# Optimization experiments

Hardware: AMD Instinct MI355X
Metric: run time of the kernel (lower is better)

Reference implementation:

```python
import jax, jax.numpy as jnp
import numpy as np
from jax import lax

N = 8192            # total ensemble boxes
W_IMG, H_IMG = 1920.0, 1080.0
NUM_MODELS = 5
CLUSTER_IOU = 0.5   # coalesce_boxes threshold


def setup_inputs() -> dict:
    key = jax.random.key(0)
    k1, k2, k3, k4, k5 = jax.random.split(key, 5)
    x1 = jax.random.uniform(k1, (N,)) * (W_IMG - 60.0)
    y1 = jax.random.uniform(k2, (N,)) * (H_IMG - 60.0)
    w = jax.random.uniform(k3, (N,)) * 180.0 + 4.0
    h = jax.random.uniform(k4, (N,)) * 180.0 + 4.0
    boxes = jnp.stack([x1, y1, x1 + w, y1 + h], axis=1)          # [N,4] xyxy
    scores = jax.random.uniform(k5, (N,)) * 0.7 + 0.3            # conf_thres=0.3
    return {"boxes": boxes, "scores": scores, "num_models": NUM_MODELS}


def _edf_forward(boxes, scores, num_models):
    n = boxes.shape[0]
    # clip to image (original also rounds; rounding omitted to keep grads alive)
    x1 = jnp.clip(boxes[:, 0], 0.0, W_IMG)
    y1 = jnp.clip(boxes[:, 1], 0.0, H_IMG)
    x2 = jnp.clip(boxes[:, 2], 0.0, W_IMG)
    y2 = jnp.clip(boxes[:, 3], 0.0, H_IMG)
    # coalesce_boxes processes boxes in descending score order (sort asc, pop)
    order = jnp.argsort(-scores)
    b = jnp.stack([x1, y1, x2, y2], axis=1)[order]               # [N,4]
    s = scores[order]
    bx1, by1, bx2, by2 = b[:, 0], b[:, 1], b[:, 2], b[:, 3]
    area = (bx2 - bx1 + 1.0) * (by2 - by1 + 1.0)
    # pairwise IoU with the +1 convention of bb_intersection_over_union
    ix1 = jnp.maximum(bx1[:, None], bx1[None, :])
    iy1 = jnp.maximum(by1[:, None], by1[None, :])
    ix2 = jnp.minimum(bx2[:, None], bx2[None, :])
    iy2 = jnp.minimum(by2[:, None], by2[None, :])
    inter = jnp.maximum(ix2 - ix1 + 1.0, 0.0) * jnp.maximum(iy2 - iy1 + 1.0, 0.0)
    iou = inter / (area[:, None] + area[None, :] - inter)        # [N,N]
    adj = iou > CLUSTER_IOU
    # greedy clustering: in score order, an unassigned box becomes a cluster
    # head and absorbs every still-unassigned box with IoU(head, j) > 0.5
    def step(cluster, i):
        is_head = cluster[i] < 0
        cluster = jnp.where(is_head & (cluster < 0) & adj[i], i, cluster)
        return cluster, None
    cluster, _ = lax.scan(step, jnp.full((n,), -1, jnp.int32),
                          jnp.arange(n, dtype=jnp.int32))
    counts = jax.ops.segment_sum(jnp.ones((n,), jnp.float32), cluster, num_segments=n)
    # per-group nms() only returns pick[0]: the member with max y2 (ties -> first)
    seg_y2 = jax.ops.segment_max(by2, cluster, num_segments=n)
    idx = jnp.arange(n)
    cand = by2 >= seg_y2[cluster]
    first = jax.ops.segment_min(jnp.where(cand, idx, n), cluster, num_segments=n)
    is_pick = idx == first[cluster]
    # probFinal = sum of group scores; final score = probFinal / num_models
    prob = jax.ops.segment_sum(s, cluster, num_segments=n)
    score_out = prob[cluster] / num_models
    # 'consensus': keep group iff its size >= num_models / 3
    valid = counts >= (num_models / 3.0)
    keep = is_pick & valid[cluster]
    out = jnp.where(keep[:, None],
                    jnp.concatenate([b, score_out[:, None]], axis=1),
                    0.0)                                         # [N,5] padded
    return out, keep


def reference(boxes, scores, num_models):
    return _edf_forward(boxes, scores, num_models)
```

## Files before the change

kernel.cpp:

```cpp
#include <hip/hip_runtime.h>
#include <cstdint>

#define N 8192
#define NT 128
#define RITERS 12
typedef unsigned long long u64;
typedef unsigned int u32;

__device__ inline u64 readlane64(u64 v, int lane) {
  u32 lo = (u32)__builtin_amdgcn_readlane((int)(u32)v, lane);
  u32 hi = (u32)__builtin_amdgcn_readlane((int)(u32)(v >> 32), lane);
  return ((u64)hi << 32) | lo;
}

__global__ __launch_bounds__(256) void k_init(const float* __restrict__ scores,
                                              u64* __restrict__ keys,
                                              int* __restrict__ rank,
                                              int* __restrict__ cnt,
                                              float* __restrict__ prob,
                                              unsigned* __restrict__ y2m,
                                              int* __restrict__ first,
                                              u64* __restrict__ D,
                                              u64* __restrict__ S) {
  int i = blockIdx.x * 256 + threadIdx.x;
  if (i >= N) return;
  float sc = scores[i];
  keys[i] = ((u64)__float_as_uint(sc) << 32) | (unsigned)(0xFFFFFFFFu - (unsigned)i);
  rank[i] = 0;
  cnt[i] = 0;
  prob[i] = 0.0f;
  y2m[i] = 0u;
  first[i] = N;
  if (i < NT) { D[i] = 0ull; S[i] = 0ull; }
}

__global__ __launch_bounds__(256) void k_rank(const u64* __restrict__ keys,
                                              int* __restrict__ rank) {
  __shared__ u64 tile[1024];
  int e = blockIdx.x * 256 + threadIdx.x;
  int j0 = blockIdx.y * 1024;
  for (int t = threadIdx.x; t < 1024; t += 256) tile[t] = keys[j0 + t];
  __syncthreads();
  u64 ke = keys[e];
  int c = 0;
#pragma unroll 8
  for (int k = 0; k < 1024; ++k) c += (tile[k] > ke) ? 1 : 0;
  atomicAdd(&rank[e], c);
}

__global__ __launch_bounds__(256) void k_scatter(const float* __restrict__ boxes,
                                                 const float* __restrict__ scores,
                                                 const int* __restrict__ rank,
                                                 float* __restrict__ bx1s, float* __restrict__ by1s,
                                                 float* __restrict__ bx2s, float* __restrict__ by2s,
                                                 float* __restrict__ ss, float* __restrict__ areas) {
#pragma clang fp contract(off)
  int i = blockIdx.x * 256 + threadIdx.x;
  if (i >= N) return;
  int r = rank[i];
  float x1 = fminf(fmaxf(boxes[i * 4 + 0], 0.0f), 1920.0f);
  float y1 = fminf(fmaxf(boxes[i * 4 + 1], 0.0f), 1080.0f);
  float x2 = fminf(fmaxf(boxes[i * 4 + 2], 0.0f), 1920.0f);
  float y2 = fminf(fmaxf(boxes[i * 4 + 3], 0.0f), 1080.0f);
  bx1s[r] = x1; by1s[r] = y1; bx2s[r] = x2; by2s[r] = y2;
  ss[r] = scores[i];
  areas[r] = (x2 - x1 + 1.0f) * (y2 - y1 + 1.0f);
}

__global__ __launch_bounds__(256) void k_adj(const float* __restrict__ bx1s, const float* __restrict__ by1s,
                                             const float* __restrict__ bx2s, const float* __restrict__ by2s,
                                             const float* __restrict__ areas,
                                             u64* __restrict__ mtile,
                                             u64* __restrict__ mrow) {
#pragma clang fp contract(off)
  __shared__ float jx1[4][64], jy1[4][64], jx2[4][64], jy2[4][64], ja[4][64];
  int w = threadIdx.x >> 6, l = threadIdx.x & 63;
  int p = blockIdx.x * 4 + w;
  int gy = (int)((sqrtf(8.0f * (float)p + 1.0f) - 1.0f) * 0.5f);
  while ((gy + 1) * (gy + 2) / 2 <= p) ++gy;
  while (gy * (gy + 1) / 2 > p) --gy;
  int gx = p - gy * (gy + 1) / 2;

  int j = gx * 64 + l;
  jx1[w][l] = bx1s[j]; jy1[w][l] = by1s[j]; jx2[w][l] = bx2s[j]; jy2[w][l] = by2s[j]; ja[w][l] = areas[j];
  __syncthreads();
  int i = gy * 64 + l;
  float x1 = bx1s[i], y1 = by1s[i], x2 = bx2s[i], y2 = by2s[i], ai = areas[i];
  u64 bits = 0;
#pragma unroll 4
  for (int jj = 0; jj < 64; ++jj) {
    float ix1 = fmaxf(x1, jx1[w][jj]);
    float iy1 = fmaxf(y1, jy1[w][jj]);
    float ix2 = fminf(x2, jx2[w][jj]);
    float iy2 = fminf(y2, jy2[w][jj]);
    float iw = fmaxf(ix2 - ix1 + 1.0f, 0.0f);
    float ih = fmaxf(iy2 - iy1 + 1.0f, 0.0f);
    float inter = iw * ih;
    float uni = (ai + ja[w][jj]) - inter;
    float t = inter + inter;
    bool gt = t > uni;
    bool amb = fabsf(t - uni) <= 1e-6f * uni;
    if (__ballot(amb) != 0ull) {
      float iou = inter / uni;
      if (amb) gt = iou > 0.5f;
    }
    bits |= ((u64)gt) << jj;
  }
  mtile[((size_t)gy * NT + gx) * 64 + l] = bits;
  mrow[(size_t)i * NT + gx] = bits;
  if (gx != gy) {
    u64 tb = 0;
#pragma unroll 8
    for (int c = 0; c < 64; ++c) {
      u64 wb = __ballot((bits >> c) & 1ull);
      tb = (l == c) ? wb : tb;
    }
    mtile[((size_t)gx * NT + gy) * 64 + l] = tb;
    mrow[(size_t)(gx * 64 + l) * NT + gy] = tb;
  }
}

__global__ __launch_bounds__(256) void k_rounds(const u64* __restrict__ mtile,
                                                u64* __restrict__ D,
                                                u64* __restrict__ S) {
  __shared__ u64 Dl[NT], Sl[NT];
  __shared__ u64 bw[3][4];
  __shared__ u64 fD, fU, fE;
  int gy = blockIdx.x;
  int t = threadIdx.x;
  int w = t >> 6, r = t & 63;
  u64 dAA = (w == 0) ? mtile[((size_t)gy * NT + gy) * 64 + r] : 0ull;

  for (int it = 0; it < RITERS; ++it) {
    if (t < NT) Dl[t] = __hip_atomic_load(&D[t], __ATOMIC_RELAXED, __HIP_MEMORY_SCOPE_AGENT);
    else Sl[t - NT] = __hip_atomic_load(&S[t - NT], __ATOMIC_RELAXED, __HIP_MEMORY_SCOPE_AGENT);
    __syncthreads();
    u64 classified = Dl[gy] | Sl[gy];
    if (classified == ~0ull) return;
    bool unk = !((classified >> r) & 1ull);
    u64 anyD = 0, anyU = 0, anyE = 0;
    if (unk) {
      int k0 = 32 * w, k1 = min(k0 + 32, gy + 1);
      for (int k = k0; k < k1; ++k) {
        u64 m = mtile[((size_t)gy * NT + k) * 64 + r];
        if (k == gy) {
          m &= (1ull << r) - 1ull;
          anyD |= m & Dl[k];
          anyU |= m & ~Sl[k];
        } else {
          anyD |= m & Dl[k];
          anyU |= m & ~Sl[k];
          anyE |= m & ~(Sl[k] | Dl[k]);
        }
      }
    }
    u64 bD = __ballot(anyD != 0ull), bU = __ballot(anyU != 0ull), bE = __ballot(anyE != 0ull);
    if (r == 0) { bw[0][w] = bD; bw[1][w] = bU; bw[2][w] = bE; }
    __syncthreads();
    if (t == 0) {
      fD = bw[0][0] | bw[0][1] | bw[0][2] | bw[0][3];
      fU = bw[1][0] | bw[1][1] | bw[1][2] | bw[1][3];
      fE = bw[2][0] | bw[2][1] | bw[2][2] | bw[2][3];
    }
    __syncthreads();
    u64 rD = fD, rU = fU, rE = fE;
    u64 unkb = ~classified;
    if (rE == 0ull) {
      if (w == 0) {
        u64 t0 = unkb & ~rD;
        u64 heads = 0, todo = t0;
        while (todo) {
          int i = __builtin_ctzll(todo);
          heads |= 1ull << i;
          todo &= ~readlane64(dAA, i);
        }
        if (r == 0) {
          if (heads) atomicOr(&D[gy], heads);
          u64 ns = unkb & ~heads;
          if (ns) atomicOr(&S[gy], ns);
        }
      }
      return;
    }
    if (t == 0) {
      u64 newS = unkb & rD;
      u64 newD = unkb & ~rD & ~rU;
      if (newS) atomicOr(&S[gy], newS);
      if (newD) atomicOr(&D[gy], newD);
    }
    __syncthreads();
  }
}

__global__ __launch_bounds__(64, 1) void k_fix(const u64* __restrict__ mrow,
                                               u64* __restrict__ D,
                                               const u64* __restrict__ S) {
  __shared__ int ulist[N];
  int l = threadIdx.x;
  u64 D0 = D[2 * l], D1 = D[2 * l + 1];
  u64 S0 = S[2 * l], S1 = S[2 * l + 1];
  u64 u0 = ~(D0 | S0), u1 = ~(D1 | S1);
  int cnt = __popcll(u0) + __popcll(u1);
  int pre = cnt;
  for (int d = 1; d < 64; d <<= 1) {
    int v = __shfl_up(pre, d);
    if (l >= d) pre += v;
  }
  int M = __shfl(pre, 63);
  int off = pre - cnt;
  {
    u64 v = u0; int o = off;
    while (v) { int b = __builtin_ctzll(v); v &= v - 1; ulist[o++] = l * 128 + b; }
    v = u1;
    while (v) { int b = __builtin_ctzll(v); v &= v - 1; ulist[o++] = l * 128 + 64 + b; }
  }
  __syncthreads();
  if (M > 0) {
    ulong2 ring[8];
    int pj[8];
#pragma unroll
    for (int q = 0; q < 8; ++q) {
      int j = ulist[q < M ? q : M - 1];
      pj[q] = j;
      ring[q] = *(const ulong2*)&mrow[(size_t)j * NT + 2 * l];
    }
    for (int m = 0; m < M; ++m) {
      int slot = m & 7;
      int j = pj[slot];
      ulong2 rv = ring[slot];
      int jt = j >> 6;
      u64 bm = (1ull << (j & 63)) - 1ull;
      u64 m0 = (2 * l < jt) ? ~0ull : ((2 * l == jt) ? bm : 0ull);
      u64 m1 = (2 * l + 1 < jt) ? ~0ull : ((2 * l + 1 == jt) ? bm : 0ull);
      bool hit = ((rv.x & D0 & m0) | (rv.y & D1 & m1)) != 0ull;
      bool head = (__ballot(hit) == 0ull);
      u64 bset = 1ull << (j & 63);
      D0 |= (head && (2 * l == jt)) ? bset : 0ull;
      D1 |= (head && (2 * l + 1 == jt)) ? bset : 0ull;
      int nm = m + 8;
      int j2 = ulist[nm < M ? nm : M - 1];
      pj[slot] = j2;
      ring[slot] = *(const ulong2*)&mrow[(size_t)j2 * NT + 2 * l];
    }
  }
  D[2 * l] = D0;
  D[2 * l + 1] = D1;
}

__global__ __launch_bounds__(256) void k_cluster(const u64* __restrict__ mtile,
                                                 const u64* __restrict__ D,
                                                 const float* __restrict__ ss,
                                                 const float* __restrict__ by2s,
                                                 int* __restrict__ cluster,
                                                 int* __restrict__ cnt,
                                                 float* __restrict__ prob,
                                                 unsigned* __restrict__ y2m) {
  __shared__ u64 hlds[NT];
  __shared__ int red[4][64];
  int gy = blockIdx.x;
  if (threadIdx.x < NT) hlds[threadIdx.x] = D[threadIdx.x];
  __syncthreads();
  int w = threadIdx.x >> 6, r = threadIdx.x & 63;
  int best = 0x7fffffff;
  for (int kk = 0; kk < 32; ++kk) {
    int k = 32 * w + kk;
    u64 v = mtile[((size_t)gy * NT + k) * 64 + r] & hlds[k];
    if (v && best == 0x7fffffff) best = k * 64 + __builtin_ctzll(v);
  }
  red[w][r] = best;
  __syncthreads();
  if (w == 0) {
    int b = min(min(red[0][r], red[1][r]), min(red[2][r], red[3][r]));
    int j = gy * 64 + r;
    cluster[j] = b;
    atomicAdd(&cnt[b], 1);
    atomicAdd(&prob[b], ss[j]);
    atomicMax(&y2m[b], __float_as_uint(by2s[j]));
  }
}

__global__ __launch_bounds__(256) void k_first(const int* __restrict__ cluster,
                                               const float* __restrict__ by2s,
                                               const unsigned* __restrict__ y2m,
                                               int* __restrict__ first) {
  int j = blockIdx.x * 256 + threadIdx.x;
  if (j >= N) return;
  int c = cluster[j];
  if (by2s[j] >= __uint_as_float(y2m[c])) atomicMin(&first[c], j);
}

__global__ __launch_bounds__(256) void k_out(const int* __restrict__ cluster,
                                             const float* __restrict__ bx1s, const float* __restrict__ by1s,
                                             const float* __restrict__ bx2s, const float* __restrict__ by2s,
                                             const int* __restrict__ cnt,
                                             const float* __restrict__ prob,
                                             const int* __restrict__ first,
                                             const int* __restrict__ num_models,
                                             float* __restrict__ out) {
  int j = blockIdx.x * 256 + threadIdx.x;
  if (j >= N) return;
  int c = cluster[j];
  int nm = num_models[0];
  bool valid = (float)cnt[c] >= (float)nm / 3.0f;
  bool pick = (first[c] == j);
  bool keep = pick && valid;
  float o0 = 0.f, o1 = 0.f, o2 = 0.f, o3 = 0.f, o4 = 0.f;
  if (keep) {
    o0 = bx1s[j]; o1 = by1s[j]; o2 = bx2s[j]; o3 = by2s[j];
    o4 = prob[c] / (float)nm;
  }
  out[j * 5 + 0] = o0;
  out[j * 5 + 1] = o1;
  out[j * 5 + 2] = o2;
  out[j * 5 + 3] = o3;
  out[j * 5 + 4] = o4;
  out[N * 5 + j] = keep ? 1.0f : 0.0f;
}

extern "C" void kernel_launch(void* const* d_in, const int* in_sizes, int n_in,
                              void* d_out, int out_size, void* d_ws, size_t ws_size,
                              hipStream_t stream) {
  const float* boxes = (const float*)d_in[0];
  const float* scores = (const float*)d_in[1];
  const int* num_models = (const int*)d_in[2];
  float* out = (float*)d_out;

  char* p = (char*)d_ws;
  auto take = [&](size_t bytes) {
    char* r = p;
    p += (bytes + 255) & ~(size_t)255;
    return r;
  };
  u64* keys   = (u64*)take((size_t)N * 8);
  int* rank   = (int*)take((size_t)N * 4);
  float* bx1s = (float*)take((size_t)N * 4);
  float* by1s = (float*)take((size_t)N * 4);
  float* bx2s = (float*)take((size_t)N * 4);
  float* by2s = (float*)take((size_t)N * 4);
  float* ss   = (float*)take((size_t)N * 4);
  float* areas= (float*)take((size_t)N * 4);
  int* cluster= (int*)take((size_t)N * 4);
  int* cnt    = (int*)take((size_t)N * 4);
  float* prob = (float*)take((size_t)N * 4);
  unsigned* y2m = (unsigned*)take((size_t)N * 4);
  int* first  = (int*)take((size_t)N * 4);
  u64* D      = (u64*)take((size_t)NT * 8);
  u64* S      = (u64*)take((size_t)NT * 8);
  u64* mtile  = (u64*)take((size_t)NT * NT * 64 * 8);
  u64* mrow   = (u64*)take((size_t)N * NT * 8);

  k_init<<<N / 256, 256, 0, stream>>>(scores, keys, rank, cnt, prob, y2m, first, D, S);
  k_rank<<<dim3(N / 256, 8), 256, 0, stream>>>(keys, rank);
  k_scatter<<<N / 256, 256, 0, stream>>>(boxes, scores, rank, bx1s, by1s, bx2s, by2s, ss, areas);
  k_adj<<<NT * (NT + 1) / 2 / 4, 256, 0, stream>>>(bx1s, by1s, bx2s, by2s, areas, mtile, mrow);
  k_rounds<<<NT, 256, 0, stream>>>(mtile, D, S);
  k_fix<<<1, 64, 0, stream>>>(mrow, D, S);
  k_cluster<<<N / 64, 256, 0, stream>>>(mtile, D, ss, by2s, cluster, cnt, prob, y2m);
  k_first<<<N / 256, 256, 0, stream>>>(cluster, by2s, y2m, first);
  k_out<<<N / 256, 256, 0, stream>>>(cluster, bx1s, by1s, bx2s, by2s, cnt, prob, first, num_models, out);
}
```

Measured before the change: 179.6 us.

## Fuse init into rank, pack y2/index max key, split rounds into launches

Merges the init and rank kernels so each thread computes its full rank over all score tiles directly, with no atomics and no keys buffer. Replaces the two-pass segment max of y2 followed by min index with a single 64-bit atomicMax on a packed (y2, inverted index) key, which removes the k_first kernel. The in-kernel iterative classification loop (12 iterations with relaxed atomic loads inside one launch) becomes 6 separate launches of a single-round kernel, so kernel boundaries provide the cross-block visibility. Fewer rounds means more unresolved work is left for the single-block k_fix pass, and each extra launch adds its own overhead.

```diff
diff --git a/kernel.cpp b/kernel.cpp
--- a/kernel.cpp
+++ b/kernel.cpp
@@ -3,7 +3,7 @@
 
 #define N 8192
 #define NT 128
-#define RITERS 12
+#define NROUNDS 6
 typedef unsigned long long u64;
 typedef unsigned int u32;
 
@@ -13,39 +13,33 @@
   return ((u64)hi << 32) | lo;
 }
 
-__global__ __launch_bounds__(256) void k_init(const float* __restrict__ scores,
-                                              u64* __restrict__ keys,
-                                              int* __restrict__ rank,
-                                              int* __restrict__ cnt,
-                                              float* __restrict__ prob,
-                                              unsigned* __restrict__ y2m,
-                                              int* __restrict__ first,
-                                              u64* __restrict__ D,
-                                              u64* __restrict__ S) {
-  int i = blockIdx.x * 256 + threadIdx.x;
-  if (i >= N) return;
-  float sc = scores[i];
-  keys[i] = ((u64)__float_as_uint(sc) << 32) | (unsigned)(0xFFFFFFFFu - (unsigned)i);
-  rank[i] = 0;
-  cnt[i] = 0;
-  prob[i] = 0.0f;
-  y2m[i] = 0u;
-  first[i] = N;
-  if (i < NT) { D[i] = 0ull; S[i] = 0ull; }
-}
-
-__global__ __launch_bounds__(256) void k_rank(const u64* __restrict__ keys,
-                                              int* __restrict__ rank) {
+__global__ __launch_bounds__(256) void k_rankz(const float* __restrict__ scores,
+                                               int* __restrict__ rank,
+                                               int* __restrict__ cnt,
+                                               float* __restrict__ prob,
+                                               u64* __restrict__ y2f,
+                                               u64* __restrict__ D,
+                                               u64* __restrict__ S) {
   __shared__ u64 tile[1024];
   int e = blockIdx.x * 256 + threadIdx.x;
-  int j0 = blockIdx.y * 1024;
-  for (int t = threadIdx.x; t < 1024; t += 256) tile[t] = keys[j0 + t];
-  __syncthreads();
-  u64 ke = keys[e];
+  u64 ke = ((u64)__float_as_uint(scores[e]) << 32) | (u32)(0xFFFFFFFFu - (u32)e);
   int c = 0;
+  for (int j0 = 0; j0 < N; j0 += 1024) {
+    __syncthreads();
+    for (int t = threadIdx.x; t < 1024; t += 256) {
+      int j = j0 + t;
+      tile[t] = ((u64)__float_as_uint(scores[j]) << 32) | (u32)(0xFFFFFFFFu - (u32)j);
+    }
+    __syncthreads();
 #pragma unroll 8
-  for (int k = 0; k < 1024; ++k) c += (tile[k] > ke) ? 1 : 0;
-  atomicAdd(&rank[e], c);
+    for (int k = 0; k < 1024; ++k) c += (tile[k] > ke) ? 1 : 0;
+  }
+  rank[e] = c;
+  cnt[e] = 0; prob[e] = 0.0f; y2f[e] = 0ull;
+  if (blockIdx.x == 0) {
+    if (threadIdx.x < NT) D[threadIdx.x] = 0ull;
+    else S[threadIdx.x - NT] = 0ull;
+  }
 }
 
 __global__ __launch_bounds__(256) void k_scatter(const float* __restrict__ boxes,
@@ -120,75 +114,65 @@
   }
 }
 
-__global__ __launch_bounds__(256) void k_rounds(const u64* __restrict__ mtile,
-                                                u64* __restrict__ D,
-                                                u64* __restrict__ S) {
+__global__ __launch_bounds__(256) void k_round(const u64* __restrict__ mtile,
+                                               u64* __restrict__ D,
+                                               u64* __restrict__ S) {
   __shared__ u64 Dl[NT], Sl[NT];
   __shared__ u64 bw[3][4];
-  __shared__ u64 fD, fU, fE;
   int gy = blockIdx.x;
   int t = threadIdx.x;
   int w = t >> 6, r = t & 63;
-  u64 dAA = (w == 0) ? mtile[((size_t)gy * NT + gy) * 64 + r] : 0ull;
-
-  for (int it = 0; it < RITERS; ++it) {
-    if (t < NT) Dl[t] = __hip_atomic_load(&D[t], __ATOMIC_RELAXED, __HIP_MEMORY_SCOPE_AGENT);
-    else Sl[t - NT] = __hip_atomic_load(&S[t - NT], __ATOMIC_RELAXED, __HIP_MEMORY_SCOPE_AGENT);
-    __syncthreads();
-    u64 classified = Dl[gy] | Sl[gy];
-    if (classified == ~0ull) return;
-    bool unk = !((classified >> r) & 1ull);
-    u64 anyD = 0, anyU = 0, anyE = 0;
-    if (unk) {
-      int k0 = 32 * w, k1 = min(k0 + 32, gy + 1);
-      for (int k = k0; k < k1; ++k) {
-        u64 m = mtile[((size_t)gy * NT + k) * 64 + r];
-        if (k == gy) {
-          m &= (1ull << r) - 1ull;
-          anyD |= m & Dl[k];
-          anyU |= m & ~Sl[k];
-        } else {
-          anyD |= m & Dl[k];
-          anyU |= m & ~Sl[k];
-          anyE |= m & ~(Sl[k] | Dl[k]);
-        }
+  if (t < NT) Dl[t] = D[t];
+  else Sl[t - NT] = S[t - NT];
+  __syncthreads();
+  u64 classified = Dl[gy] | Sl[gy];
+  if (classified == ~0ull) return;
+  bool unk = !((classified >> r) & 1ull);
+  u64 anyD = 0, anyU = 0, anyE = 0;
+  if (unk) {
+    int k0 = 32 * w, k1 = min(k0 + 32, gy + 1);
+    for (int k = k0; k < k1; ++k) {
+      u64 m = mtile[((size_t)gy * NT + k) * 64 + r];
+      if (k == gy) {
+        m &= (1ull << r) - 1ull;
+        anyD |= m & Dl[k];
+        anyU |= m & ~Sl[k];
+      } else {
+        anyD |= m & Dl[k];
+        anyU |= m & ~Sl[k];
+        anyE |= m & ~(Sl[k] | Dl[k]);
       }
     }
-    u64 bD = __ballot(anyD != 0ull), bU = __ballot(anyU != 0ull), bE = __ballot(anyE != 0ull);
-    if (r == 0) { bw[0][w] = bD; bw[1][w] = bU; bw[2][w] = bE; }
-    __syncthreads();
-    if (t == 0) {
-      fD = bw[0][0] | bw[0][1] | bw[0][2] | bw[0][3];
-      fU = bw[1][0] | bw[1][1] | bw[1][2] | bw[1][3];
-      fE = bw[2][0] | bw[2][1] | bw[2][2] | bw[2][3];
-    }
-    __syncthreads();
-    u64 rD = fD, rU = fU, rE = fE;
-    u64 unkb = ~classified;
-    if (rE == 0ull) {
-      if (w == 0) {
-        u64 t0 = unkb & ~rD;
-        u64 heads = 0, todo = t0;
-        while (todo) {
-          int i = __builtin_ctzll(todo);
-          heads |= 1ull << i;
-          todo &= ~readlane64(dAA, i);
-        }
-        if (r == 0) {
-          if (heads) atomicOr(&D[gy], heads);
-          u64 ns = unkb & ~heads;
-          if (ns) atomicOr(&S[gy], ns);
-        }
+  }
+  u64 bD = __ballot(anyD != 0ull), bU = __ballot(anyU != 0ull), bE = __ballot(anyE != 0ull);
+  if (r == 0) { bw[0][w] = bD; bw[1][w] = bU; bw[2][w] = bE; }
+  __syncthreads();
+  u64 rD = bw[0][0] | bw[0][1] | bw[0][2] | bw[0][3];
+  u64 rU = bw[1][0] | bw[1][1] | bw[1][2] | bw[1][3];
+  u64 rE = bw[2][0] | bw[2][1] | bw[2][2] | bw[2][3];
+  u64 unkb = ~classified;
+  if (rE == 0ull) {
+    if (w == 0) {
+      u64 dAA = mtile[((size_t)gy * NT + gy) * 64 + r];
+      u64 heads = 0, todo = unkb & ~rD;
+      while (todo) {
+        int i = __builtin_ctzll(todo);
+        heads |= 1ull << i;
+        todo &= ~readlane64(dAA, i);
       }
-      return;
-    }
-    if (t == 0) {
-      u64 newS = unkb & rD;
-      u64 newD = unkb & ~rD & ~rU;
-      if (newS) atomicOr(&S[gy], newS);
-      if (newD) atomicOr(&D[gy], newD);
-    }
-    __syncthreads();
+      if (r == 0) {
+        if (heads) atomicOr(&D[gy], heads);
+        u64 ns = unkb & ~heads;
+        if (ns) atomicOr(&S[gy], ns);
+      }
+    }
+    return;
+  }
+  if (t == 0) {
+    u64 newS = unkb & rD;
+    u64 newD = unkb & ~rD & ~rU;
+    if (newS) atomicOr(&S[gy], newS);
+    if (newD) atomicOr(&D[gy], newD);
   }
 }
 
@@ -254,7 +238,7 @@
                                                  int* __restrict__ cluster,
                                                  int* __restrict__ cnt,
                                                  float* __restrict__ prob,
-                                                 unsigned* __restrict__ y2m) {
+                                                 u64* __restrict__ y2f) {
   __shared__ u64 hlds[NT];
   __shared__ int red[4][64];
   int gy = blockIdx.x;
@@ -275,18 +259,9 @@
     cluster[j] = b;
     atomicAdd(&cnt[b], 1);
     atomicAdd(&prob[b], ss[j]);
-    atomicMax(&y2m[b], __float_as_uint(by2s[j]));
-  }
-}
-
-__global__ __launch_bounds__(256) void k_first(const int* __restrict__ cluster,
-                                               const float* __restrict__ by2s,
-                                               const unsigned* __restrict__ y2m,
-                                               int* __restrict__ first) {
-  int j = blockIdx.x * 256 + threadIdx.x;
-  if (j >= N) return;
-  int c = cluster[j];
-  if (by2s[j] >= __uint_as_float(y2m[c])) atomicMin(&first[c], j);
+    u64 key = ((u64)__float_as_uint(by2s[j]) << 32) | (u32)(0xFFFFFFFFu - (u32)j);
+    atomicMax(&y2f[b], key);
+  }
 }
 
 __global__ __launch_bounds__(256) void k_out(const int* __restrict__ cluster,
@@ -294,7 +269,7 @@
                                              const float* __restrict__ bx2s, const float* __restrict__ by2s,
                                              const int* __restrict__ cnt,
                                              const float* __restrict__ prob,
-                                             const int* __restrict__ first,
+                                             const u64* __restrict__ y2f,
                                              const int* __restrict__ num_models,
                                              float* __restrict__ out) {
   int j = blockIdx.x * 256 + threadIdx.x;
@@ -302,8 +277,8 @@
   int c = cluster[j];
   int nm = num_models[0];
   bool valid = (float)cnt[c] >= (float)nm / 3.0f;
-  bool pick = (first[c] == j);
-  bool keep = pick && valid;
+  int jf = (int)(0xFFFFFFFFu - (u32)(y2f[c] & 0xFFFFFFFFull));
+  bool keep = (jf == j) && valid;
   float o0 = 0.f, o1 = 0.f, o2 = 0.f, o3 = 0.f, o4 = 0.f;
   if (keep) {
     o0 = bx1s[j]; o1 = by1s[j]; o2 = bx2s[j]; o3 = by2s[j];
@@ -331,7 +306,6 @@
     p += (bytes + 255) & ~(size_t)255;
     return r;
   };
-  u64* keys   = (u64*)take((size_t)N * 8);
   int* rank   = (int*)take((size_t)N * 4);
   float* bx1s = (float*)take((size_t)N * 4);
   float* by1s = (float*)take((size_t)N * 4);
@@ -342,20 +316,18 @@
   int* cluster= (int*)take((size_t)N * 4);
   int* cnt    = (int*)take((size_t)N * 4);
   float* prob = (float*)take((size_t)N * 4);
-  unsigned* y2m = (unsigned*)take((size_t)N * 4);
-  int* first  = (int*)take((size_t)N * 4);
+  u64* y2f    = (u64*)take((size_t)N * 8);
   u64* D      = (u64*)take((size_t)NT * 8);
   u64* S      = (u64*)take((size_t)NT * 8);
   u64* mtile  = (u64*)take((size_t)NT * NT * 64 * 8);
   u64* mrow   = (u64*)take((size_t)N * NT * 8);
 
-  k_init<<<N / 256, 256, 0, stream>>>(scores, keys, rank, cnt, prob, y2m, first, D, S);
-  k_rank<<<dim3(N / 256, 8), 256, 0, stream>>>(keys, rank);
+  k_rankz<<<N / 256, 256, 0, stream>>>(scores, rank, cnt, prob, y2f, D, S);
   k_scatter<<<N / 256, 256, 0, stream>>>(boxes, scores, rank, bx1s, by1s, bx2s, by2s, ss, areas);
   k_adj<<<NT * (NT + 1) / 2 / 4, 256, 0, stream>>>(bx1s, by1s, bx2s, by2s, areas, mtile, mrow);
-  k_rounds<<<NT, 256, 0, stream>>>(mtile, D, S);
+  for (int r = 0; r < NROUNDS; ++r)
+    k_round<<<NT, 256, 0, stream>>>(mtile, D, S);
   k_fix<<<1, 64, 0, stream>>>(mrow, D, S);
-  k_cluster<<<N / 64, 256, 0, stream>>>(mtile, D, ss, by2s, cluster, cnt, prob, y2m);
-  k_first<<<N / 256, 256, 0, stream>>>(cluster, by2s, y2m, first);
-  k_out<<<N / 256, 256, 0, stream>>>(cluster, bx1s, by1s, bx2s, by2s, cnt, prob, first, num_models, out);
-}
+  k_cluster<<<N / 64, 256, 0, stream>>>(mtile, D, ss, by2s, cluster, cnt, prob, y2f);
+  k_out<<<N / 256, 256, 0, stream>>>(cluster, bx1s, by1s, bx2s, by2s, cnt, prob, y2f, num_models, out);
+}
```

Result: slower. 272.9 us (+51.9%).
